# Optimization experiments

Hardware: AMD Instinct MI355X
Metric: run time of the kernel (lower is better)

## Reference

```python
import jax, jax.numpy as jnp
import numpy as np
from jax import lax

NEG_INF = -10000.0
START_LABEL = 1  # '[CLS]'
STOP_LABEL = 2   # '[SEP]'


def setup_inputs() -> dict:
    key = jax.random.key(0)
    k1, k2, k3, k4 = jax.random.split(key, 4)
    B, T, H, L = 64, 512, 768, 10
    hidden = jax.random.normal(k1, (B, T, H), dtype=jnp.float32)
    W = jax.random.normal(k2, (L, H), dtype=jnp.float32) * (1.0 / np.sqrt(H))
    b = jnp.zeros((L,), dtype=jnp.float32)
    transitions = jax.random.normal(k3, (L, L), dtype=jnp.float32)
    transitions = transitions.at[START_LABEL, :].set(NEG_INF)
    transitions = transitions.at[:, STOP_LABEL].set(NEG_INF)
    label_ids = jax.random.randint(k4, (B, T), 0, L, dtype=jnp.int64)
    return {"hidden": hidden, "W": W, "b": b, "transitions": transitions,
            "label_ids": label_ids}


def _logsumexp(x, axis=-1):
    m = jnp.max(x, axis=axis, keepdims=True)
    return jnp.squeeze(m, axis) + jnp.log(jnp.sum(jnp.exp(x - m), axis=axis))


def reference(hidden, W, b, transitions, label_ids):
    # hidden: [B, T, H]; emission features [B, T, L]
    feats = jnp.einsum('bth,lh->btl', hidden, W) + b
    B, T, L = feats.shape

    # ---- CRF forward algorithm (partition function) ----
    alpha0 = jnp.full((B, L), NEG_INF, dtype=feats.dtype).at[:, START_LABEL].set(0.0)

    def step(alpha, feat_t):
        # transitions[i, j] + alpha[:, j] -> [B, L(next), L(prev)]
        scores = transitions[None, :, :] + alpha[:, None, :]
        new_alpha = _logsumexp(scores, axis=-1) + feat_t  # [B, L]
        return new_alpha, None

    feats_seq = jnp.swapaxes(feats[:, 1:], 0, 1)  # [T-1, B, L]
    alpha, _ = lax.scan(step, alpha0, feats_seq)
    forward_score = _logsumexp(alpha, axis=-1)  # [B]

    # ---- gold score ----
    prev = label_ids[:, :-1]  # [B, T-1]
    cur = label_ids[:, 1:]    # [B, T-1]
    trans_score = transitions[cur, prev].sum(axis=-1)  # [B]
    emit_score = jnp.take_along_axis(feats[:, 1:], cur[..., None], axis=-1)[..., 0].sum(axis=-1)
    gold_score = trans_score + emit_score  # [B]

    return jnp.mean(forward_score - gold_score)
```

## Files before the change

kernel.cpp:

```cpp
#include <hip/hip_runtime.h>
#include <hip/hip_bf16.h>


#define NL 10
#define TL 512
#define HDIM 768
#define CS 16
#define NCHUNK 32
#define LOG2E_F 1.4426950408889634f
#define LN2_F 0.6931471805599453f

__global__ __launch_bounds__(128, 2) void crf_chunk(
    const float* __restrict__ hidden, const float* __restrict__ W,
    const float* __restrict__ bias, const float* __restrict__ trans,
    const int* __restrict__ labels, float* __restrict__ Pmats,
    float* __restrict__ Cc, float* __restrict__ golds)
{
  const int tid = threadIdx.x;
  const int w = tid >> 6;
  const int lane = tid & 63;
  const int c = blockIdx.x * 2 + w;
  const int b = blockIdx.y;
  const int r = lane & 15;
  const int q = lane >> 4;
  const int t = c * CS + 1 + r;
  const bool valid = (t < TL);
  const int tc = valid ? t : (TL - 1);

  __shared__ float4 sW[1920];
  __shared__ float sE[2][CS][12];

#pragma unroll
  for (int i = 0; i < 15; ++i) {
    const int idx = i * 128 + tid;
    sW[idx] = ((const float4*)W)[idx];
  }
  __syncthreads();

  float acc[NL];
#pragma unroll
  for (int l = 0; l < NL; ++l) acc[l] = 0.0f;

  const float4* __restrict__ h4 =
      (const float4*)(hidden + ((size_t)b * TL + tc) * HDIM) + q;
#pragma unroll 8
  for (int j = 0; j < 48; ++j) {
    const float4 h = h4[j * 4];
#pragma unroll
    for (int l = 0; l < NL; ++l) {
      const float4 wv = sW[l * 192 + j * 4 + q];
      acc[l] += h.x * wv.x + h.y * wv.y + h.z * wv.z + h.w * wv.w;
    }
  }
#pragma unroll
  for (int l = 0; l < NL; ++l) {
    acc[l] += __shfl_xor(acc[l], 16);
    acc[l] += __shfl_xor(acc[l], 32);
    acc[l] += bias[l];
  }

  float g = 0.0f;
  if (lane < CS) {
#pragma unroll
    for (int l = 0; l < NL; ++l)
      sE[w][r][l] = valid ? exp2f(acc[l] * LOG2E_F) : 0.0f;
    if (valid) {
      const int cu = labels[b * TL + t];
      const int pv = labels[b * TL + t - 1];
      float emit = 0.0f;
#pragma unroll
      for (int l = 0; l < NL; ++l) emit = (cu == l) ? acc[l] : emit;
      g = emit + trans[cu * NL + pv];
    }
  }
#pragma unroll
  for (int off = 32; off; off >>= 1) g += __shfl_down(g, off);
  if (lane == 0) golds[b * NCHUNK + c] = g;

  __syncthreads();

  const int ep = lane % NL;

  float Tm[NL][NL];
#pragma unroll
  for (int el = 0; el < NL; ++el)
#pragma unroll
    for (int k = 0; k < NL; ++k)
      Tm[el][k] = exp2f(trans[el * NL + k] * LOG2E_F);

  float p[NL];
#pragma unroll
  for (int el = 0; el < NL; ++el) p[el] = sE[w][0][el] * Tm[el][ep];

  const int NT = (c == NCHUNK - 1) ? (CS - 1) : CS;
  float Cacc = 0.0f;

  for (int s = 1; s < NT; ++s) {
    const float* __restrict__ se = &sE[w][s][0];
    float pn[NL];
#pragma unroll
    for (int el = 0; el < NL; ++el) {
      float sum = Tm[el][0] * p[0];
#pragma unroll
      for (int k = 1; k < NL; ++k) sum += Tm[el][k] * p[k];
      pn[el] = se[el] * sum;
    }
#pragma unroll
    for (int el = 0; el < NL; ++el) p[el] = pn[el];

    if ((s & 3) == 3 || s == NT - 1) {
      float m = p[0];
#pragma unroll
      for (int el = 1; el < NL; ++el) m = fmaxf(m, p[el]);
#pragma unroll
      for (int off = 1; off < 64; off <<= 1) m = fmaxf(m, __shfl_xor(m, off));
      m = fmaxf(m, 1e-33f);
      const float e = floorf(log2f(m));
      const float scl = exp2f(-e);
      Cacc += e;
#pragma unroll
      for (int el = 0; el < NL; ++el) p[el] *= scl;
    }
  }

  float* __restrict__ Pb = Pmats + (size_t)(b * NCHUNK + c) * 100;
  if (lane < NL) {
#pragma unroll
    for (int el = 0; el < NL; ++el) Pb[el * NL + ep] = p[el];
  }
  if (lane == 0) Cc[b * NCHUNK + c] = Cacc;
}

__global__ __launch_bounds__(64, 2) void crf_combine(
    const float* __restrict__ Pmats, const float* __restrict__ Cc,
    const float* __restrict__ golds, float* __restrict__ out)
{
  const int b = blockIdx.x;
  const int lane = threadIdx.x;
  const int el = lane % NL;

  __shared__ float sP[NCHUNK * 100];

  const float* __restrict__ src = Pmats + (size_t)b * (NCHUNK * 100);
#pragma unroll
  for (int i = 0; i < (NCHUNK * 100) / 64; ++i)
    sP[i * 64 + lane] = src[i * 64 + lane];

  float cg = (lane < NCHUNK) ? Cc[b * NCHUNK + lane] : 0.0f;
  float gg = (lane < NCHUNK) ? golds[b * NCHUNK + lane] : 0.0f;
#pragma unroll
  for (int off = 16; off; off >>= 1) {
    cg += __shfl_down(cg, off);
    gg += __shfl_down(gg, off);
  }
  float C = __shfl(cg, 0);
  const float gold = __shfl(gg, 0);

  __syncthreads();

  float v[NL];
#pragma unroll
  for (int p = 0; p < NL; ++p) v[p] = sP[p * NL + 1];

  float bufA[NL], bufB[NL];
#pragma unroll
  for (int k = 0; k < NL; ++k) bufA[k] = sP[1 * 100 + el * NL + k];

  for (int c = 1; c < NCHUNK; c += 2) {
    const int cn = (c + 1 < NCHUNK) ? (c + 1) : c;
#pragma unroll
    for (int k = 0; k < NL; ++k) bufB[k] = sP[cn * 100 + el * NL + k];

    float nv = bufA[0] * v[0];
#pragma unroll
    for (int k = 1; k < NL; ++k) nv += bufA[k] * v[k];
#pragma unroll
    for (int p = 0; p < NL; ++p) v[p] = __shfl(nv, p);

    if (c + 1 < NCHUNK) {
      const int cn2 = (c + 2 < NCHUNK) ? (c + 2) : (c + 1);
#pragma unroll
      for (int k = 0; k < NL; ++k) bufA[k] = sP[cn2 * 100 + el * NL + k];

      float nv2 = bufB[0] * v[0];
#pragma unroll
      for (int k = 1; k < NL; ++k) nv2 += bufB[k] * v[k];
#pragma unroll
      for (int p = 0; p < NL; ++p) v[p] = __shfl(nv2, p);

      float m = v[0];
#pragma unroll
      for (int p = 1; p < NL; ++p) m = fmaxf(m, v[p]);
      m = fmaxf(m, 1e-33f);
      const float e = floorf(log2f(m));
      const float scl = exp2f(-e);
      C += e;
#pragma unroll
      for (int p = 0; p < NL; ++p) v[p] *= scl;
    }
  }

  float s = 0.0f;
#pragma unroll
  for (int p = 0; p < NL; ++p) s += v[p];
  const float fwd = LN2_F * (log2f(s) + C);
  if (lane == 0) atomicAdd(out, (fwd - gold) * (1.0f / 64.0f));
}

extern "C" void kernel_launch(void* const* d_in, const int* in_sizes, int n_in,
                              void* d_out, int out_size, void* d_ws, size_t ws_size,
                              hipStream_t stream) {
  const float* hidden = (const float*)d_in[0];
  const float* W      = (const float*)d_in[1];
  const float* bias   = (const float*)d_in[2];
  const float* trans  = (const float*)d_in[3];
  const int*   labels = (const int*)d_in[4];

  float* ws    = (float*)d_ws;
  float* Pmats = ws;
  float* Cc    = ws + 64 * NCHUNK * 100;
  float* golds = Cc + 64 * NCHUNK;

  hipMemsetAsync(d_out, 0, sizeof(float), stream);

  dim3 grid1(NCHUNK / 2, 64);
  crf_chunk<<<grid1, 128, 0, stream>>>(hidden, W, bias, trans, labels,
                                       Pmats, Cc, golds);
  crf_combine<<<64, 64, 0, stream>>>(Pmats, Cc, golds, (float*)d_out);
}
```

Before: 197.0 us.

## Split emission GEMV into its own kernel and shorten CRF chain chunks

Moves the hidden·W emission projection into a separate bandwidth-oriented kernel where each thread handles two rows with coalesced float4 loads, and writes exp(emissions) to workspace. A new chain kernel then computes per-chunk transfer matrices with chunk size halved (64 chunks of 8), and the combine kernel multiplies 64 matrices instead of 32. The aim is better memory throughput for the dominant 100MB read and a shorter serial recurrence per chunk. The cost is an extra kernel launch, an intermediate round-trip through global memory, and a longer serial matrix chain in combine.

Result: slower. 212.6 us (+7.9%).

```diff
diff --git a/kernel.cpp b/kernel.cpp
--- a/kernel.cpp
+++ b/kernel.cpp
@@ -5,78 +5,124 @@
 #define NL 10
 #define TL 512
 #define HDIM 768
-#define CS 16
-#define NCHUNK 32
+#define CS 8
+#define NCHUNK 64
+#define NB 64
 #define LOG2E_F 1.4426950408889634f
 #define LN2_F 0.6931471805599453f
 
-__global__ __launch_bounds__(128, 2) void crf_chunk(
+__global__ __launch_bounds__(256, 4) void crf_feats(
     const float* __restrict__ hidden, const float* __restrict__ W,
     const float* __restrict__ bias, const float* __restrict__ trans,
-    const int* __restrict__ labels, float* __restrict__ Pmats,
-    float* __restrict__ Cc, float* __restrict__ golds)
+    const int* __restrict__ labels, float* __restrict__ E,
+    float* __restrict__ golds2)
 {
   const int tid = threadIdx.x;
   const int w = tid >> 6;
   const int lane = tid & 63;
-  const int c = blockIdx.x * 2 + w;
+  const int rs = lane >> 4;
+  const int q = lane & 15;
+  const int row0 = blockIdx.x * 32 + w * 8 + rs;
+  const int row1 = row0 + 4;
+
+  __shared__ float4 sW[1920];
+  __shared__ float sGold[4];
+
+  for (int i = tid; i < 1920; i += 256)
+    sW[i] = ((const float4*)W)[i];
+  __syncthreads();
+
+  float acc0[NL], acc1[NL];
+#pragma unroll
+  for (int l = 0; l < NL; ++l) { acc0[l] = 0.0f; acc1[l] = 0.0f; }
+
+  const float4* __restrict__ h4 = (const float4*)hidden;
+  const size_t b0 = (size_t)row0 * 192;
+  const size_t b1 = (size_t)row1 * 192;
+
+#pragma unroll
+  for (int half = 0; half < 2; ++half) {
+    float4 hA[6], hB[6];
+#pragma unroll
+    for (int j = 0; j < 6; ++j) {
+      const int f4i = (half * 6 + j) * 16 + q;
+      hA[j] = h4[b0 + f4i];
+      hB[j] = h4[b1 + f4i];
+    }
+#pragma unroll
+    for (int j = 0; j < 6; ++j) {
+      const int f4i = (half * 6 + j) * 16 + q;
+#pragma unroll
+      for (int l = 0; l < NL; ++l) {
+        const float4 wv = sW[l * 192 + f4i];
+        acc0[l] += hA[j].x * wv.x + hA[j].y * wv.y + hA[j].z * wv.z + hA[j].w * wv.w;
+        acc1[l] += hB[j].x * wv.x + hB[j].y * wv.y + hB[j].z * wv.z + hB[j].w * wv.w;
+      }
+    }
+  }
+
+#pragma unroll
+  for (int l = 0; l < NL; ++l) {
+#pragma unroll
+    for (int off = 1; off < 16; off <<= 1) {
+      acc0[l] += __shfl_xor(acc0[l], off);
+      acc1[l] += __shfl_xor(acc1[l], off);
+    }
+    const float bl = bias[l];
+    acc0[l] += bl; acc1[l] += bl;
+  }
+
+  if (q < NL) {
+    float s0 = acc0[0], s1 = acc1[0];
+#pragma unroll
+    for (int l = 1; l < NL; ++l) {
+      s0 = (q == l) ? acc0[l] : s0;
+      s1 = (q == l) ? acc1[l] : s1;
+    }
+    E[(size_t)row0 * NL + q] = exp2f(s0 * LOG2E_F);
+    E[(size_t)row1 * NL + q] = exp2f(s1 * LOG2E_F);
+  }
+
+  float g = 0.0f;
+  if (q == 0) {
+    if ((row0 & (TL - 1)) > 0) {
+      const int cu = labels[row0], pv = labels[row0 - 1];
+      float emit = acc0[0];
+#pragma unroll
+      for (int l = 1; l < NL; ++l) emit = (cu == l) ? acc0[l] : emit;
+      g += emit + trans[cu * NL + pv];
+    }
+    {
+      const int cu = labels[row1], pv = labels[row1 - 1];
+      float emit = acc1[0];
+#pragma unroll
+      for (int l = 1; l < NL; ++l) emit = (cu == l) ? acc1[l] : emit;
+      g += emit + trans[cu * NL + pv];
+    }
+  }
+  g += __shfl_xor(g, 16);
+  g += __shfl_xor(g, 32);
+  if (lane == 0) sGold[w] = g;
+  __syncthreads();
+  if (tid == 0)
+    golds2[blockIdx.x] = sGold[0] + sGold[1] + sGold[2] + sGold[3];
+}
+
+__global__ __launch_bounds__(64) void crf_chain(
+    const float* __restrict__ E, const float* __restrict__ trans,
+    float* __restrict__ Pmats, float* __restrict__ Cc)
+{
+  const int c = blockIdx.x;
   const int b = blockIdx.y;
-  const int r = lane & 15;
-  const int q = lane >> 4;
-  const int t = c * CS + 1 + r;
-  const bool valid = (t < TL);
-  const int tc = valid ? t : (TL - 1);
-
-  __shared__ float4 sW[1920];
-  __shared__ float sE[2][CS][12];
-
-#pragma unroll
-  for (int i = 0; i < 15; ++i) {
-    const int idx = i * 128 + tid;
-    sW[idx] = ((const float4*)W)[idx];
-  }
-  __syncthreads();
-
-  float acc[NL];
-#pragma unroll
-  for (int l = 0; l < NL; ++l) acc[l] = 0.0f;
-
-  const float4* __restrict__ h4 =
-      (const float4*)(hidden + ((size_t)b * TL + tc) * HDIM) + q;
-#pragma unroll 8
-  for (int j = 0; j < 48; ++j) {
-    const float4 h = h4[j * 4];
-#pragma unroll
-    for (int l = 0; l < NL; ++l) {
-      const float4 wv = sW[l * 192 + j * 4 + q];
-      acc[l] += h.x * wv.x + h.y * wv.y + h.z * wv.z + h.w * wv.w;
-    }
-  }
-#pragma unroll
-  for (int l = 0; l < NL; ++l) {
-    acc[l] += __shfl_xor(acc[l], 16);
-    acc[l] += __shfl_xor(acc[l], 32);
-    acc[l] += bias[l];
-  }
-
-  float g = 0.0f;
-  if (lane < CS) {
-#pragma unroll
-    for (int l = 0; l < NL; ++l)
-      sE[w][r][l] = valid ? exp2f(acc[l] * LOG2E_F) : 0.0f;
-    if (valid) {
-      const int cu = labels[b * TL + t];
-      const int pv = labels[b * TL + t - 1];
-      float emit = 0.0f;
-#pragma unroll
-      for (int l = 0; l < NL; ++l) emit = (cu == l) ? acc[l] : emit;
-      g = emit + trans[cu * NL + pv];
-    }
-  }
-#pragma unroll
-  for (int off = 32; off; off >>= 1) g += __shfl_down(g, off);
-  if (lane == 0) golds[b * NCHUNK + c] = g;
-
+  const int lane = threadIdx.x;
+  const int t0 = c * CS + 1;
+  const int NT = (c == NCHUNK - 1) ? (CS - 1) : CS;
+
+  __shared__ float sEl[CS * NL];
+
+  const float* __restrict__ src = E + (size_t)(b * TL + t0) * NL;
+  const int n = NT * NL;
+  for (int i = lane; i < n; i += 64) sEl[i] = src[i];
   __syncthreads();
 
   const int ep = lane % NL;
@@ -90,20 +136,17 @@
 
   float p[NL];
 #pragma unroll
-  for (int el = 0; el < NL; ++el) p[el] = sE[w][0][el] * Tm[el][ep];
-
-  const int NT = (c == NCHUNK - 1) ? (CS - 1) : CS;
+  for (int el = 0; el < NL; ++el) p[el] = sEl[el] * Tm[el][ep];
+
   float Cacc = 0.0f;
-
   for (int s = 1; s < NT; ++s) {
-    const float* __restrict__ se = &sE[w][s][0];
     float pn[NL];
 #pragma unroll
     for (int el = 0; el < NL; ++el) {
       float sum = Tm[el][0] * p[0];
 #pragma unroll
       for (int k = 1; k < NL; ++k) sum += Tm[el][k] * p[k];
-      pn[el] = se[el] * sum;
+      pn[el] = sEl[s * NL + el] * sum;
     }
 #pragma unroll
     for (int el = 0; el < NL; ++el) p[el] = pn[el];
@@ -126,30 +169,30 @@
   float* __restrict__ Pb = Pmats + (size_t)(b * NCHUNK + c) * 100;
   if (lane < NL) {
 #pragma unroll
-    for (int el = 0; el < NL; ++el) Pb[el * NL + ep] = p[el];
+    for (int el = 0; el < NL; ++el) Pb[el * NL + lane] = p[el];
   }
   if (lane == 0) Cc[b * NCHUNK + c] = Cacc;
 }
 
 __global__ __launch_bounds__(64, 2) void crf_combine(
     const float* __restrict__ Pmats, const float* __restrict__ Cc,
-    const float* __restrict__ golds, float* __restrict__ out)
+    const float* __restrict__ golds2, float* __restrict__ out)
 {
   const int b = blockIdx.x;
   const int lane = threadIdx.x;
   const int el = lane % NL;
 
-  __shared__ float sP[NCHUNK * 100];
-
-  const float* __restrict__ src = Pmats + (size_t)b * (NCHUNK * 100);
-#pragma unroll
-  for (int i = 0; i < (NCHUNK * 100) / 64; ++i)
-    sP[i * 64 + lane] = src[i * 64 + lane];
-
-  float cg = (lane < NCHUNK) ? Cc[b * NCHUNK + lane] : 0.0f;
-  float gg = (lane < NCHUNK) ? golds[b * NCHUNK + lane] : 0.0f;
-#pragma unroll
-  for (int off = 16; off; off >>= 1) {
+  __shared__ float4 sP4[1600];
+  float* sP = (float*)sP4;
+
+  const float4* __restrict__ src = (const float4*)(Pmats + (size_t)b * 6400);
+#pragma unroll
+  for (int i = 0; i < 25; ++i) sP4[i * 64 + lane] = src[i * 64 + lane];
+
+  float cg = Cc[b * NCHUNK + lane];
+  float gg = (lane < 16) ? golds2[b * 16 + lane] : 0.0f;
+#pragma unroll
+  for (int off = 32; off; off >>= 1) {
     cg += __shfl_down(cg, off);
     gg += __shfl_down(gg, off);
   }
@@ -216,15 +259,15 @@
   const float* trans  = (const float*)d_in[3];
   const int*   labels = (const int*)d_in[4];
 
-  float* ws    = (float*)d_ws;
-  float* Pmats = ws;
-  float* Cc    = ws + 64 * NCHUNK * 100;
-  float* golds = Cc + 64 * NCHUNK;
+  float* ws     = (float*)d_ws;
+  float* E      = ws;
+  float* Pmats  = E + 327680;
+  float* Cc     = Pmats + 409600;
+  float* golds2 = Cc + 4096;
 
   hipMemsetAsync(d_out, 0, sizeof(float), stream);
 
-  dim3 grid1(NCHUNK / 2, 64);
-  crf_chunk<<<grid1, 128, 0, stream>>>(hidden, W, bias, trans, labels,
-                                       Pmats, Cc, golds);
-  crf_combine<<<64, 64, 0, stream>>>(Pmats, Cc, golds, (float*)d_out);
-}
+  crf_feats<<<1024, 256, 0, stream>>>(hidden, W, bias, trans, labels, E, golds2);
+  crf_chain<<<dim3(NCHUNK, NB), 64, 0, stream>>>(E, trans, Pmats, Cc);
+  crf_combine<<<NB, 64, 0, stream>>>(Pmats, Cc, golds2, (float*)d_out);
+}
```
